# Kernel optimization log

Measured on AMD Instinct MI355X. Metric: run time of the kernel, lower is better.

## Reference

```python
import jax, jax.numpy as jnp
import numpy as np

T, H, I, E, TOP_K = 2048, 1024, 768, 8, 2


def setup_inputs() -> dict:
    key = jax.random.key(0)
    kx, kg, ku, kd, kr = jax.random.split(key, 5)
    scale_h = 1.0 / np.sqrt(H)
    scale_i = 1.0 / np.sqrt(I)
    x = jax.random.normal(kx, (T, H), dtype=jnp.float32)
    gate_w = jax.random.normal(kg, (E, I, H), dtype=jnp.float32) * scale_h
    up_w = jax.random.normal(ku, (E, I, H), dtype=jnp.float32) * scale_h
    down_w = jax.random.normal(kd, (E, H, I), dtype=jnp.float32) * scale_i
    # Router: top-k over random logits, softmax over selected, scatter to dense [T, E]
    logits = jax.random.normal(kr, (T, E), dtype=jnp.float32)
    top_vals, top_idx = jax.lax.top_k(logits, TOP_K)          # [T, K]
    top_w = jax.nn.softmax(top_vals, axis=-1)                 # [T, K]
    rows = jnp.arange(T)[:, None]                             # [T, 1]
    masked_routing_weights = jnp.zeros((T, E), jnp.float32).at[rows, top_idx].set(top_w)
    expert_select_count = jnp.zeros((E,), jnp.int32).at[top_idx.reshape(-1)].add(1)
    return {
        "x": x,
        "gate_w": gate_w,
        "up_w": up_w,
        "down_w": down_w,
        "masked_routing_weights": masked_routing_weights,
        "expert_select_count": expert_select_count,
    }


def reference(x, gate_w, up_w, down_w, masked_routing_weights, expert_select_count):
    # custom_moe_glu: per-expert GLU MLP, combined with masked routing weights.
    # x: [T, H]; gate_w/up_w: [E, I, H]; down_w: [E, H, I]; routing: [T, E]
    g = jnp.einsum("th,eih->tei", x, gate_w)                  # [T, E, I]
    u = jnp.einsum("th,eih->tei", x, up_w)                    # [T, E, I]
    h = jax.nn.silu(g) * u                                    # fused GLU activation
    # down projection per expert, then weighted combine over experts
    out = jnp.einsum("tei,ehi,te->th", h, down_w, masked_routing_weights)
    return out
```

## Files before the change

### kernel.cpp

```cpp
#include <hip/hip_runtime.h>
#include <hip/hip_bf16.h>

#define T_TOK 2048
#define H_DIM 1024
#define I_DIM 768
#define NEXP  8
#define WPE   6291456

typedef short bf16x8  __attribute__((ext_vector_type(8)));
typedef short short4v __attribute__((ext_vector_type(4)));
typedef float f32x4   __attribute__((ext_vector_type(4)));

__device__ __forceinline__ short f2bf(float f) {
  __bf16 b = (__bf16)f;
  return __builtin_bit_cast(short, b);
}
__device__ __forceinline__ void gload16(const void* g, void* l) {
  __builtin_amdgcn_global_load_lds(
      (const __attribute__((address_space(1))) void*)g,
      (__attribute__((address_space(3))) void*)l, 16, 0, 0);
}
__device__ __forceinline__ int padcnt(int c) { return (c + 127) & ~127; }
__device__ __forceinline__ int ebase(const int* __restrict__ cnts, int e) {
  int b = 0;
#pragma unroll
  for (int i = 0; i < NEXP; ++i)
    if (i < e) b += padcnt(cnts[i]);
  return b;
}


__global__ __launch_bounds__(512) void compact_k(const float* __restrict__ routw,
                                                 int* __restrict__ wsI) {
  __shared__ int sc[8];
  int e = blockIdx.x, lane = threadIdx.x & 63, w = threadIdx.x >> 6;
  unsigned long long mk[4];
  int cnt = 0;
#pragma unroll
  for (int c = 0; c < 4; ++c) {
    int tk = w * 256 + c * 64 + lane;
    float v = routw[(size_t)tk * NEXP + e];
    mk[c] = __ballot(v > 0.f);
    cnt += __popcll(mk[c]);
  }
  if (lane == 0) sc[w] = cnt;
  __syncthreads();
  int run = 0;
#pragma unroll
  for (int j = 0; j < 8; ++j)
    if (j < w) run += sc[j];
#pragma unroll
  for (int c = 0; c < 4; ++c) {
    int tk = w * 256 + c * 64 + lane;
    if ((mk[c] >> lane) & 1ull) {
      int pos = __popcll(mk[c] & ((1ull << lane) - 1));
      wsI[64 + e * T_TOK + run + pos] = tk;
    }
    run += __popcll(mk[c]);
  }
  if (w == 7 && lane == 0) wsI[e] = run;
}

__global__ __launch_bounds__(256) void gatherconv_k(const float* __restrict__ x,
                                                    const float* __restrict__ gw,
                                                    const float* __restrict__ uw,
                                                    const int* __restrict__ wsI,
                                                    unsigned short* __restrict__ xc,
                                                    unsigned short* __restrict__ wbf) {
  int bid = blockIdx.x;
  if (bid < 4096) {
    int e = bid >> 9, rb = bid & 511;
    int cnt = wsI[e];
    int pad = padcnt(cnt);
    int r = rb * 4 + (threadIdx.x >> 6);
    if (r >= pad) return;
    int base = ebase(wsI, e);
    int col = (threadIdx.x & 63) * 16;
    unsigned short* dst = xc + (size_t)(base + r) * H_DIM + col;
    if (r < cnt) {
      int tok = wsI[64 + e * T_TOK + r];
      const float* sr = x + (size_t)tok * H_DIM + col;
#pragma unroll
      for (int j = 0; j < 4; ++j) {
        float4 v = *(const float4*)(sr + j * 4);
        short4v b = {f2bf(v.x), f2bf(v.y), f2bf(v.z), f2bf(v.w)};
        *(short4v*)(dst + j * 4) = b;
      }
    } else {
#pragma unroll
      for (int j = 0; j < 4; ++j) {
        short4v z = {0, 0, 0, 0};
        *(short4v*)(dst + j * 4) = z;
      }
    }
  } else {
    size_t off = ((size_t)(bid - 4096) * 256 + threadIdx.x) * 16;
    int a = (off >= (size_t)WPE) ? 1 : 0;
    size_t rem = off - (size_t)a * WPE;
    const float* s = (a ? uw : gw) + rem;
    unsigned short* o = wbf + (size_t)a * WPE + rem;
#pragma unroll
    for (int j = 0; j < 4; ++j) {
      float4 v = *(const float4*)(s + j * 4);
      short4v b = {f2bf(v.x), f2bf(v.y), f2bf(v.z), f2bf(v.w)};
      *(short4v*)(o + j * 4) = b;
    }
  }
}

#define WB(v)                                              \
  do {                                                     \
    asm volatile("s_waitcnt vmcnt(" #v ")" ::: "memory");  \
    __builtin_amdgcn_s_barrier();                          \
    __builtin_amdgcn_sched_barrier(0);                     \
  } while (0)

__global__ __launch_bounds__(512, 2) void gemm1_k(
    const unsigned short* __restrict__ xc, unsigned short* __restrict__ wbf,
    const int* __restrict__ wsI, unsigned short* __restrict__ h,
    const float* __restrict__ dw, float* __restrict__ out) {
  int bid = blockIdx.x;
  if (bid >= 768) {
    if (bid < 1536) {
      size_t off = ((size_t)(bid - 768) * 512 + threadIdx.x) * 16;
      const float* s = dw + off;
      unsigned short* o = wbf + 2 * (size_t)WPE + off;
#pragma unroll
      for (int j = 0; j < 4; ++j) {
        float4 v = *(const float4*)(s + j * 4);
        short4v b = {f2bf(v.x), f2bf(v.y), f2bf(v.z), f2bf(v.w)};
        *(short4v*)(o + j * 4) = b;
      }
    } else {
      size_t off = ((size_t)(bid - 1536) * 512 + threadIdx.x) * 16;
      f32x4 z = {0.f, 0.f, 0.f, 0.f};
#pragma unroll
      for (int j = 0; j < 4; ++j) *(f32x4*)(out + off + j * 4) = z;
    }
    return;
  }
  int e = bid & 7, rr = bid >> 3;
  int mt = rr & 15, nt = rr >> 4;
  int cnt = wsI[e];
  int m0 = mt * 128;
  if (m0 >= cnt) return;
  int base = ebase(wsI, e);
  int n0 = nt * 128;

  __shared__ unsigned short ls[5][12288];

  int tid = threadIdx.x, lane = tid & 63, w = tid >> 6;
  int wm = w >> 2, wn = w & 3;
  int fr = lane & 15, fg = lane >> 4;
  int srow = lane >> 2;
  int scol = ((lane & 3) ^ (srow & 3)) * 8;

  const unsigned short* srcA = xc + (size_t)(base + m0 + 16 * w + srow) * H_DIM + scol;
  const unsigned short* srcG = wbf + (size_t)(e * I_DIM + n0 + 16 * w + srow) * H_DIM + scol;
  const unsigned short* srcU = wbf + WPE + (size_t)(e * I_DIM + n0 + 16 * w + srow) * H_DIM + scol;

  int roA[4], roB[4];
#pragma unroll
  for (int m = 0; m < 4; ++m) {
    int r2 = wm * 64 + m * 16 + fr;
    roA[m] = r2 * 32 + ((fg ^ (r2 & 3)) << 3);
  }
#pragma unroll
  for (int n = 0; n < 4; ++n) {
    int r2 = (n < 2) ? (wn * 32 + n * 16 + fr) : (128 + wn * 32 + (n - 2) * 16 + fr);
    roB[n] = 4096 + r2 * 32 + ((fg ^ (r2 & 3)) << 3);
  }

  bf16x8 af[2][4], bv[2][4];
  f32x4 acc[4][4] = {};

#define STG1(hh)                                                     \
  do {                                                               \
    unsigned short* lb = &ls[(hh) % 5][0];                           \
    gload16(srcA + (hh) * 32, lb + w * 512);                         \
    gload16(srcG + (hh) * 32, lb + 4096 + w * 512);                  \
    gload16(srcU + (hh) * 32, lb + 4096 + (w + 8) * 512);            \
  } while (0)
#define LDF1(st, hh)                                                 \
  do {                                                               \
    const unsigned short* lb = &ls[(hh) % 5][0];                     \
    _Pragma("unroll") for (int m = 0; m < 4; ++m) af[st][m] = *(const bf16x8*)(lb + roA[m]); \
    _Pragma("unroll") for (int n = 0; n < 4; ++n) bv[st][n] = *(const bf16x8*)(lb + roB[n]); \
  } while (0)
#define MM1(st)                                                      \
  do {                                                               \
    __builtin_amdgcn_s_setprio(1);                                   \
    _Pragma("unroll") for (int m = 0; m < 4; ++m)                    \
      _Pragma("unroll") for (int n = 0; n < 4; ++n)                  \
        acc[m][n] = __builtin_amdgcn_mfma_f32_16x16x32_bf16(af[st][m], bv[st][n], acc[m][n], 0, 0, 0); \
    __builtin_amdgcn_s_setprio(0);                                   \
  } while (0)

  STG1(0); STG1(1); STG1(2); STG1(3);
  WB(6);
  LDF1(0, 0);
#pragma unroll
  for (int i = 0; i < 32; ++i) {
    if (i + 4 < 32) STG1(i + 4);
    if (i + 1 < 32) LDF1((i + 1) & 1, i + 1);
    MM1(i & 1);
    if (i <= 27)      WB(6);
    else if (i == 28) WB(3);
    else if (i == 29) WB(0);
  }
#undef STG1
#undef LDF1
#undef MM1

#pragma unroll
  for (int m = 0; m < 4; ++m)
#pragma unroll
    for (int j = 0; j < 4; ++j) {
      int row = wm * 64 + m * 16 + fg * 4 + j;
      size_t rb2 = (size_t)(base + m0 + row) * I_DIM + n0;
#pragma unroll
      for (int jn = 0; jn < 2; ++jn) {
        float g = acc[m][jn][j];
        float u = acc[m][jn + 2][j];
        h[rb2 + wn * 32 + jn * 16 + fr] = (unsigned short)f2bf(g * u / (1.f + __expf(-g)));
      }
    }
}

__global__ __launch_bounds__(512, 2) void gemm2_k(
    const unsigned short* __restrict__ h, const unsigned short* __restrict__ wbf,
    const int* __restrict__ wsI, const float* __restrict__ routw,
    float* __restrict__ out) {
  int e = blockIdx.x & 7, rr = blockIdx.x >> 3;
  int mt = rr & 15, nt = rr >> 4;
  int cnt = wsI[e];
  int m0 = mt * 128;
  if (m0 >= cnt) return;
  int base = ebase(wsI, e);
  int n0 = nt * 256;
  const unsigned short* down_bf = wbf + 2 * (size_t)WPE;

  __shared__ unsigned short ls[5][12288];

  int tid = threadIdx.x, lane = tid & 63, w = tid >> 6;
  int wm = w >> 2, wn = w & 3;
  int fr = lane & 15, fg = lane >> 4;
  int srow = lane >> 2;
  int scol = ((lane & 3) ^ (srow & 3)) * 8;

  const unsigned short* srcA  = h + (size_t)(base + m0 + 16 * w + srow) * I_DIM + scol;
  const unsigned short* srcB1 = down_bf + (size_t)(e * H_DIM + n0 + 16 * w + srow) * I_DIM + scol;
  const unsigned short* srcB2 = down_bf + (size_t)(e * H_DIM + n0 + 16 * (w + 8) + srow) * I_DIM + scol;

  int roA[4], roB[4];
#pragma unroll
  for (int m = 0; m < 4; ++m) {
    int r2 = wm * 64 + m * 16 + fr;
    roA[m] = r2 * 32 + ((fg ^ (r2 & 3)) << 3);
  }
#pragma unroll
  for (int n = 0; n < 4; ++n) {
    int r2 = wn * 64 + n * 16 + fr;
    roB[n] = 4096 + r2 * 32 + ((fg ^ (r2 & 3)) << 3);
  }

  bf16x8 af[2][4], bv[2][4];
  f32x4 acc[4][4] = {};

#define STG2(hh)                                                     \
  do {                                                               \
    unsigned short* lb = &ls[(hh) % 5][0];                           \
    gload16(srcA + (hh) * 32, lb + w * 512);                         \
    gload16(srcB1 + (hh) * 32, lb + 4096 + w * 512);                 \
    gload16(srcB2 + (hh) * 32, lb + 4096 + (w + 8) * 512);           \
  } while (0)
#define LDF2(st, hh)                                                 \
  do {                                                               \
    const unsigned short* lb = &ls[(hh) % 5][0];                     \
    _Pragma("unroll") for (int m = 0; m < 4; ++m) af[st][m] = *(const bf16x8*)(lb + roA[m]); \
    _Pragma("unroll") for (int n = 0; n < 4; ++n) bv[st][n] = *(const bf16x8*)(lb + roB[n]); \
  } while (0)
#define MM2(st)                                                      \
  do {                                                               \
    __builtin_amdgcn_s_setprio(1);                                   \
    _Pragma("unroll") for (int m = 0; m < 4; ++m)                    \
      _Pragma("unroll") for (int n = 0; n < 4; ++n)                  \
        acc[m][n] = __builtin_amdgcn_mfma_f32_16x16x32_bf16(af[st][m], bv[st][n], acc[m][n], 0, 0, 0); \
    __builtin_amdgcn_s_setprio(0);                                   \
  } while (0)

  STG2(0); STG2(1); STG2(2); STG2(3);
  WB(6);
  LDF2(0, 0);
#pragma unroll
  for (int i = 0; i < 24; ++i) {
    if (i + 4 < 24) STG2(i + 4);
    if (i + 1 < 24) LDF2((i + 1) & 1, i + 1);
    MM2(i & 1);
    if (i <= 19)      WB(6);
    else if (i == 20) WB(3);
    else if (i == 21) WB(0);
  }
#undef STG2
#undef LDF2
#undef MM2

#pragma unroll
  for (int m = 0; m < 4; ++m)
#pragma unroll
    for (int j = 0; j < 4; ++j) {
      int row = wm * 64 + m * 16 + fg * 4 + j;
      int grow = m0 + row;
      if (grow < cnt) {
        int tk = wsI[64 + e * T_TOK + grow];
        float rw = routw[(size_t)tk * NEXP + e];
        float* orow = out + (size_t)tk * H_DIM + n0 + wn * 64;
#pragma unroll
        for (int n = 0; n < 4; ++n)
          atomicAdd(orow + n * 16 + fr, acc[m][n][j] * rw);
      }
    }
}

extern "C" void kernel_launch(void* const* d_in, const int* in_sizes, int n_in,
                              void* d_out, int out_size, void* d_ws, size_t ws_size,
                              hipStream_t stream) {
  const float* x      = (const float*)d_in[0];
  const float* gate_w = (const float*)d_in[1];
  const float* up_w   = (const float*)d_in[2];
  const float* down_w = (const float*)d_in[3];
  const float* routw  = (const float*)d_in[4];
  float* out = (float*)d_out;
  int* wsI = (int*)d_ws;

  unsigned short* wbf = (unsigned short*)((char*)d_ws + 131072);
  unsigned short* xc  = (unsigned short*)((char*)d_ws + 37879808);
  unsigned short* h   = (unsigned short*)((char*)d_ws + 48365568);

  compact_k<<<8, 512, 0, stream>>>(routw, wsI);
  gatherconv_k<<<7168, 256, 0, stream>>>(x, gate_w, up_w, wsI, xc, wbf);
  gemm1_k<<<1792, 512, 0, stream>>>(xc, wbf, wsI, h, down_w, out);
  gemm2_k<<<512, 512, 0, stream>>>(h, wbf, wsI, routw, out);
}
```

Measured before the change: 87.19 us.

## Shrink GEMM tiles to 64 rows with 2-wave blocks and simple double buffering

Both expert GEMMs move from 512-thread blocks with 128-row tiles and a 5-stage LDS pipeline to 128-thread blocks with 64-row tiles and a two-buffer loop synchronised by __syncthreads. Expert padding drops from 128 to 64 rows, which cuts wasted work on padded rows and gives more blocks to fill the GPU. The LDS swizzle gains an extra XOR term to reduce bank conflicts. In exchange the shallower pipeline and smaller tiles give less latency hiding and less operand reuse per block, and the extra blocks add more global traffic.

```diff
diff --git a/kernel.cpp b/kernel.cpp
--- a/kernel.cpp
+++ b/kernel.cpp
@@ -20,13 +20,16 @@
       (const __attribute__((address_space(1))) void*)g,
       (__attribute__((address_space(3))) void*)l, 16, 0, 0);
 }
-__device__ __forceinline__ int padcnt(int c) { return (c + 127) & ~127; }
+__device__ __forceinline__ int padcnt(int c) { return (c + 63) & ~63; }
 __device__ __forceinline__ int ebase(const int* __restrict__ cnts, int e) {
   int b = 0;
 #pragma unroll
   for (int i = 0; i < NEXP; ++i)
     if (i < e) b += padcnt(cnts[i]);
   return b;
+}
+__device__ __forceinline__ int swz(int row, int g) {
+  return g ^ (row & 3) ^ ((row >> 2) & 1);
 }
 
 
@@ -108,21 +111,15 @@
   }
 }
 
-#define WB(v)                                              \
-  do {                                                     \
-    asm volatile("s_waitcnt vmcnt(" #v ")" ::: "memory");  \
-    __builtin_amdgcn_s_barrier();                          \
-    __builtin_amdgcn_sched_barrier(0);                     \
-  } while (0)
-
-__global__ __launch_bounds__(512, 2) void gemm1_k(
+__global__ __launch_bounds__(128, 3) void gemm1_k(
     const unsigned short* __restrict__ xc, unsigned short* __restrict__ wbf,
     const int* __restrict__ wsI, unsigned short* __restrict__ h,
     const float* __restrict__ dw, float* __restrict__ out) {
   int bid = blockIdx.x;
-  if (bid >= 768) {
-    if (bid < 1536) {
-      size_t off = ((size_t)(bid - 768) * 512 + threadIdx.x) * 16;
+  int tid = threadIdx.x;
+  if (bid >= 3072) {
+    if (bid < 6144) {
+      size_t off = ((size_t)(bid - 3072) * 128 + tid) * 16;
       const float* s = dw + off;
       unsigned short* o = wbf + 2 * (size_t)WPE + off;
 #pragma unroll
@@ -132,7 +129,7 @@
         *(short4v*)(o + j * 4) = b;
       }
     } else {
-      size_t off = ((size_t)(bid - 1536) * 512 + threadIdx.x) * 16;
+      size_t off = ((size_t)(bid - 6144) * 128 + tid) * 16;
       f32x4 z = {0.f, 0.f, 0.f, 0.f};
 #pragma unroll
       for (int j = 0; j < 4; ++j) *(f32x4*)(out + off + j * 4) = z;
@@ -140,181 +137,183 @@
     return;
   }
   int e = bid & 7, rr = bid >> 3;
-  int mt = rr & 15, nt = rr >> 4;
+  int mt = rr & 31, nt = rr >> 5;
   int cnt = wsI[e];
-  int m0 = mt * 128;
+  int m0 = mt * 64;
   if (m0 >= cnt) return;
   int base = ebase(wsI, e);
-  int n0 = nt * 128;
-
-  __shared__ unsigned short ls[5][12288];
-
-  int tid = threadIdx.x, lane = tid & 63, w = tid >> 6;
-  int wm = w >> 2, wn = w & 3;
+  int g0 = nt * 64;
+
+  __shared__ unsigned short ls[2][6144];
+
+  int lane = tid & 63, w = tid >> 6;
   int fr = lane & 15, fg = lane >> 4;
   int srow = lane >> 2;
-  int scol = ((lane & 3) ^ (srow & 3)) * 8;
-
-  const unsigned short* srcA = xc + (size_t)(base + m0 + 16 * w + srow) * H_DIM + scol;
-  const unsigned short* srcG = wbf + (size_t)(e * I_DIM + n0 + 16 * w + srow) * H_DIM + scol;
-  const unsigned short* srcU = wbf + WPE + (size_t)(e * I_DIM + n0 + 16 * w + srow) * H_DIM + scol;
+  int scol = swz(srow, lane & 3) * 8;
+
+  const unsigned short* gate_bf = wbf;
+  const unsigned short* up_bf   = wbf + WPE;
+
+  const unsigned short* srcA[2];
+  const unsigned short* srcB[4];
+  int ldA[2], ldB[4];
+#pragma unroll
+  for (int i = 0; i < 2; ++i) {
+    int c = w + 2 * i;
+    ldA[i] = c * 512;
+    srcA[i] = xc + (size_t)(base + m0 + 16 * c + srow) * H_DIM + scol;
+  }
+#pragma unroll
+  for (int i = 0; i < 4; ++i) {
+    int c = w + 2 * i;
+    ldB[i] = 2048 + c * 512;
+    srcB[i] = ((c < 4) ? gate_bf + (size_t)(e * I_DIM + g0 + 16 * c + srow) * H_DIM
+                       : up_bf   + (size_t)(e * I_DIM + g0 + 16 * (c - 4) + srow) * H_DIM) + scol;
+  }
 
   int roA[4], roB[4];
 #pragma unroll
   for (int m = 0; m < 4; ++m) {
-    int r2 = wm * 64 + m * 16 + fr;
-    roA[m] = r2 * 32 + ((fg ^ (r2 & 3)) << 3);
+    int r2 = m * 16 + fr;
+    roA[m] = r2 * 32 + (swz(r2, fg) << 3);
   }
 #pragma unroll
   for (int n = 0; n < 4; ++n) {
-    int r2 = (n < 2) ? (wn * 32 + n * 16 + fr) : (128 + wn * 32 + (n - 2) * 16 + fr);
-    roB[n] = 4096 + r2 * 32 + ((fg ^ (r2 & 3)) << 3);
-  }
-
-  bf16x8 af[2][4], bv[2][4];
+    int r2 = (n < 2) ? (w * 32 + n * 16 + fr) : (64 + w * 32 + (n - 2) * 16 + fr);
+    roB[n] = 2048 + r2 * 32 + (swz(r2, fg) << 3);
+  }
+
   f32x4 acc[4][4] = {};
 
-#define STG1(hh)                                                     \
-  do {                                                               \
-    unsigned short* lb = &ls[(hh) % 5][0];                           \
-    gload16(srcA + (hh) * 32, lb + w * 512);                         \
-    gload16(srcG + (hh) * 32, lb + 4096 + w * 512);                  \
-    gload16(srcU + (hh) * 32, lb + 4096 + (w + 8) * 512);            \
+#define STG1(buf, k)                                        \
+  do {                                                      \
+    _Pragma("unroll") for (int i = 0; i < 2; ++i)           \
+      gload16(srcA[i] + (k) * 32, &ls[buf][ldA[i]]);        \
+    _Pragma("unroll") for (int i = 0; i < 4; ++i)           \
+      gload16(srcB[i] + (k) * 32, &ls[buf][ldB[i]]);        \
   } while (0)
-#define LDF1(st, hh)                                                 \
-  do {                                                               \
-    const unsigned short* lb = &ls[(hh) % 5][0];                     \
-    _Pragma("unroll") for (int m = 0; m < 4; ++m) af[st][m] = *(const bf16x8*)(lb + roA[m]); \
-    _Pragma("unroll") for (int n = 0; n < 4; ++n) bv[st][n] = *(const bf16x8*)(lb + roB[n]); \
-  } while (0)
-#define MM1(st)                                                      \
-  do {                                                               \
-    __builtin_amdgcn_s_setprio(1);                                   \
-    _Pragma("unroll") for (int m = 0; m < 4; ++m)                    \
-      _Pragma("unroll") for (int n = 0; n < 4; ++n)                  \
-        acc[m][n] = __builtin_amdgcn_mfma_f32_16x16x32_bf16(af[st][m], bv[st][n], acc[m][n], 0, 0, 0); \
-    __builtin_amdgcn_s_setprio(0);                                   \
-  } while (0)
-
-  STG1(0); STG1(1); STG1(2); STG1(3);
-  WB(6);
-  LDF1(0, 0);
-#pragma unroll
-  for (int i = 0; i < 32; ++i) {
-    if (i + 4 < 32) STG1(i + 4);
-    if (i + 1 < 32) LDF1((i + 1) & 1, i + 1);
-    MM1(i & 1);
-    if (i <= 27)      WB(6);
-    else if (i == 28) WB(3);
-    else if (i == 29) WB(0);
+
+  STG1(0, 0);
+  __syncthreads();
+  for (int k = 0; k < 32; ++k) {
+    int cur = k & 1;
+    if (k + 1 < 32) STG1(cur ^ 1, k + 1);
+    bf16x8 af[4], bv[4];
+#pragma unroll
+    for (int m = 0; m < 4; ++m) af[m] = *(const bf16x8*)&ls[cur][roA[m]];
+#pragma unroll
+    for (int n = 0; n < 4; ++n) bv[n] = *(const bf16x8*)&ls[cur][roB[n]];
+#pragma unroll
+    for (int m = 0; m < 4; ++m)
+#pragma unroll
+      for (int n = 0; n < 4; ++n)
+        acc[m][n] = __builtin_amdgcn_mfma_f32_16x16x32_bf16(af[m], bv[n], acc[m][n], 0, 0, 0);
+    __syncthreads();
   }
 #undef STG1
-#undef LDF1
-#undef MM1
 
 #pragma unroll
   for (int m = 0; m < 4; ++m)
 #pragma unroll
     for (int j = 0; j < 4; ++j) {
-      int row = wm * 64 + m * 16 + fg * 4 + j;
-      size_t rb2 = (size_t)(base + m0 + row) * I_DIM + n0;
+      int row = m * 16 + fg * 4 + j;
+      size_t rb2 = (size_t)(base + m0 + row) * I_DIM + g0;
 #pragma unroll
       for (int jn = 0; jn < 2; ++jn) {
         float g = acc[m][jn][j];
         float u = acc[m][jn + 2][j];
-        h[rb2 + wn * 32 + jn * 16 + fr] = (unsigned short)f2bf(g * u / (1.f + __expf(-g)));
-      }
-    }
-}
-
-__global__ __launch_bounds__(512, 2) void gemm2_k(
+        h[rb2 + w * 32 + jn * 16 + fr] = (unsigned short)f2bf(g * u / (1.f + __expf(-g)));
+      }
+    }
+}
+
+__global__ __launch_bounds__(128, 3) void gemm2_k(
     const unsigned short* __restrict__ h, const unsigned short* __restrict__ wbf,
     const int* __restrict__ wsI, const float* __restrict__ routw,
     float* __restrict__ out) {
   int e = blockIdx.x & 7, rr = blockIdx.x >> 3;
-  int mt = rr & 15, nt = rr >> 4;
+  int mt = rr & 31, nt = rr >> 5;
   int cnt = wsI[e];
-  int m0 = mt * 128;
+  int m0 = mt * 64;
   if (m0 >= cnt) return;
   int base = ebase(wsI, e);
-  int n0 = nt * 256;
+  int n0 = nt * 128;
   const unsigned short* down_bf = wbf + 2 * (size_t)WPE;
 
-  __shared__ unsigned short ls[5][12288];
+  __shared__ unsigned short ls[2][6144];
 
   int tid = threadIdx.x, lane = tid & 63, w = tid >> 6;
-  int wm = w >> 2, wn = w & 3;
   int fr = lane & 15, fg = lane >> 4;
   int srow = lane >> 2;
-  int scol = ((lane & 3) ^ (srow & 3)) * 8;
-
-  const unsigned short* srcA  = h + (size_t)(base + m0 + 16 * w + srow) * I_DIM + scol;
-  const unsigned short* srcB1 = down_bf + (size_t)(e * H_DIM + n0 + 16 * w + srow) * I_DIM + scol;
-  const unsigned short* srcB2 = down_bf + (size_t)(e * H_DIM + n0 + 16 * (w + 8) + srow) * I_DIM + scol;
+  int scol = swz(srow, lane & 3) * 8;
+
+  const unsigned short* srcA[2];
+  const unsigned short* srcB[4];
+  int ldA[2], ldB[4];
+#pragma unroll
+  for (int i = 0; i < 2; ++i) {
+    int c = w + 2 * i;
+    ldA[i] = c * 512;
+    srcA[i] = h + (size_t)(base + m0 + 16 * c + srow) * I_DIM + scol;
+  }
+#pragma unroll
+  for (int i = 0; i < 4; ++i) {
+    int c = w + 2 * i;
+    ldB[i] = 2048 + c * 512;
+    srcB[i] = down_bf + (size_t)(e * H_DIM + n0 + 16 * c + srow) * I_DIM + scol;
+  }
 
   int roA[4], roB[4];
 #pragma unroll
   for (int m = 0; m < 4; ++m) {
-    int r2 = wm * 64 + m * 16 + fr;
-    roA[m] = r2 * 32 + ((fg ^ (r2 & 3)) << 3);
+    int r2 = m * 16 + fr;
+    roA[m] = r2 * 32 + (swz(r2, fg) << 3);
   }
 #pragma unroll
   for (int n = 0; n < 4; ++n) {
-    int r2 = wn * 64 + n * 16 + fr;
-    roB[n] = 4096 + r2 * 32 + ((fg ^ (r2 & 3)) << 3);
-  }
-
-  bf16x8 af[2][4], bv[2][4];
+    int r2 = w * 64 + n * 16 + fr;
+    roB[n] = 2048 + r2 * 32 + (swz(r2, fg) << 3);
+  }
+
   f32x4 acc[4][4] = {};
 
-#define STG2(hh)                                                     \
-  do {                                                               \
-    unsigned short* lb = &ls[(hh) % 5][0];                           \
-    gload16(srcA + (hh) * 32, lb + w * 512);                         \
-    gload16(srcB1 + (hh) * 32, lb + 4096 + w * 512);                 \
-    gload16(srcB2 + (hh) * 32, lb + 4096 + (w + 8) * 512);           \
+#define STG2(buf, k)                                        \
+  do {                                                      \
+    _Pragma("unroll") for (int i = 0; i < 2; ++i)           \
+      gload16(srcA[i] + (k) * 32, &ls[buf][ldA[i]]);        \
+    _Pragma("unroll") for (int i = 0; i < 4; ++i)           \
+      gload16(srcB[i] + (k) * 32, &ls[buf][ldB[i]]);        \
   } while (0)
-#define LDF2(st, hh)                                                 \
-  do {                                                               \
-    const unsigned short* lb = &ls[(hh) % 5][0];                     \
-    _Pragma("unroll") for (int m = 0; m < 4; ++m) af[st][m] = *(const bf16x8*)(lb + roA[m]); \
-    _Pragma("unroll") for (int n = 0; n < 4; ++n) bv[st][n] = *(const bf16x8*)(lb + roB[n]); \
-  } while (0)
-#define MM2(st)                                                      \
-  do {                                                               \
-    __builtin_amdgcn_s_setprio(1);                                   \
-    _Pragma("unroll") for (int m = 0; m < 4; ++m)                    \
-      _Pragma("unroll") for (int n = 0; n < 4; ++n)                  \
-        acc[m][n] = __builtin_amdgcn_mfma_f32_16x16x32_bf16(af[st][m], bv[st][n], acc[m][n], 0, 0, 0); \
-    __builtin_amdgcn_s_setprio(0);                                   \
-  } while (0)
-
-  STG2(0); STG2(1); STG2(2); STG2(3);
-  WB(6);
-  LDF2(0, 0);
-#pragma unroll
-  for (int i = 0; i < 24; ++i) {
-    if (i + 4 < 24) STG2(i + 4);
-    if (i + 1 < 24) LDF2((i + 1) & 1, i + 1);
-    MM2(i & 1);
-    if (i <= 19)      WB(6);
-    else if (i == 20) WB(3);
-    else if (i == 21) WB(0);
+
+  STG2(0, 0);
+  __syncthreads();
+  for (int k = 0; k < 24; ++k) {
+    int cur = k & 1;
+    if (k + 1 < 24) STG2(cur ^ 1, k + 1);
+    bf16x8 af[4], bv[4];
+#pragma unroll
+    for (int m = 0; m < 4; ++m) af[m] = *(const bf16x8*)&ls[cur][roA[m]];
+#pragma unroll
+    for (int n = 0; n < 4; ++n) bv[n] = *(const bf16x8*)&ls[cur][roB[n]];
+#pragma unroll
+    for (int m = 0; m < 4; ++m)
+#pragma unroll
+      for (int n = 0; n < 4; ++n)
+        acc[m][n] = __builtin_amdgcn_mfma_f32_16x16x32_bf16(af[m], bv[n], acc[m][n], 0, 0, 0);
+    __syncthreads();
   }
 #undef STG2
-#undef LDF2
-#undef MM2
 
 #pragma unroll
   for (int m = 0; m < 4; ++m)
 #pragma unroll
     for (int j = 0; j < 4; ++j) {
-      int row = wm * 64 + m * 16 + fg * 4 + j;
+      int row = m * 16 + fg * 4 + j;
       int grow = m0 + row;
       if (grow < cnt) {
         int tk = wsI[64 + e * T_TOK + grow];
         float rw = routw[(size_t)tk * NEXP + e];
-        float* orow = out + (size_t)tk * H_DIM + n0 + wn * 64;
+        float* orow = out + (size_t)tk * H_DIM + n0 + w * 64;
 #pragma unroll
         for (int n = 0; n < 4; ++n)
           atomicAdd(orow + n * 16 + fr, acc[m][n][j] * rw);
@@ -339,6 +338,6 @@
 
   compact_k<<<8, 512, 0, stream>>>(routw, wsI);
   gatherconv_k<<<7168, 256, 0, stream>>>(x, gate_w, up_w, wsI, xc, wbf);
-  gemm1_k<<<1792, 512, 0, stream>>>(xc, wbf, wsI, h, down_w, out);
-  gemm2_k<<<512, 512, 0, stream>>>(h, wbf, wsI, routw, out);
-}
+  gemm1_k<<<7168, 128, 0, stream>>>(xc, wbf, wsI, h, down_w, out);
+  gemm2_k<<<2048, 128, 0, stream>>>(h, wbf, wsI, routw, out);
+}
```

After: 98.47 us. 12.9% more time.

## Move down-weight conversion and output zeroing into pre-kernel; refine LDS swizzle

Applied to the files above, without the earlier changes.

The down_w fp32-to-bf16 conversion and the zeroing of the output move out of the gemm1 launch (extra blocks) and into the preprocessing kernel, so gemm1 launches only its 768 GEMM tiles. The LDS XOR swizzle gains an extra bit from the row index (bit 2), which is meant to cut bank conflicts on fragment reads in both GEMMs. The tradeoff is a longer pre-kernel on the critical path, where before that conversion work overlapped with gemm1's compute blocks.

```diff
diff --git a/kernel.cpp b/kernel.cpp
--- a/kernel.cpp
+++ b/kernel.cpp
@@ -61,21 +61,23 @@
   if (w == 7 && lane == 0) wsI[e] = run;
 }
 
-__global__ __launch_bounds__(256) void gatherconv_k(const float* __restrict__ x,
-                                                    const float* __restrict__ gw,
-                                                    const float* __restrict__ uw,
-                                                    const int* __restrict__ wsI,
-                                                    unsigned short* __restrict__ xc,
-                                                    unsigned short* __restrict__ wbf) {
-  int bid = blockIdx.x;
+__global__ __launch_bounds__(256) void pre_k(const float* __restrict__ x,
+                                             const float* __restrict__ gw,
+                                             const float* __restrict__ uw,
+                                             const float* __restrict__ dw,
+                                             const int* __restrict__ wsI,
+                                             unsigned short* __restrict__ xc,
+                                             unsigned short* __restrict__ wbf,
+                                             float* __restrict__ out) {
+  int bid = blockIdx.x, tid = threadIdx.x;
   if (bid < 4096) {
     int e = bid >> 9, rb = bid & 511;
     int cnt = wsI[e];
     int pad = padcnt(cnt);
-    int r = rb * 4 + (threadIdx.x >> 6);
+    int r = rb * 4 + (tid >> 6);
     if (r >= pad) return;
     int base = ebase(wsI, e);
-    int col = (threadIdx.x & 63) * 16;
+    int col = (tid & 63) * 16;
     unsigned short* dst = xc + (size_t)(base + r) * H_DIM + col;
     if (r < cnt) {
       int tok = wsI[64 + e * T_TOK + r];
@@ -93,11 +95,11 @@
         *(short4v*)(dst + j * 4) = z;
       }
     }
-  } else {
-    size_t off = ((size_t)(bid - 4096) * 256 + threadIdx.x) * 16;
-    int a = (off >= (size_t)WPE) ? 1 : 0;
+  } else if (bid < 8704) {
+    size_t off = ((size_t)(bid - 4096) * 256 + tid) * 16;
+    int a = (int)(off / (size_t)WPE);
     size_t rem = off - (size_t)a * WPE;
-    const float* s = (a ? uw : gw) + rem;
+    const float* s = ((a == 0) ? gw : (a == 1) ? uw : dw) + rem;
     unsigned short* o = wbf + (size_t)a * WPE + rem;
 #pragma unroll
     for (int j = 0; j < 4; ++j) {
@@ -105,6 +107,11 @@
       short4v b = {f2bf(v.x), f2bf(v.y), f2bf(v.z), f2bf(v.w)};
       *(short4v*)(o + j * 4) = b;
     }
+  } else {
+    size_t off = ((size_t)(bid - 8704) * 256 + tid) * 16;
+    f32x4 z = {0.f, 0.f, 0.f, 0.f};
+#pragma unroll
+    for (int j = 0; j < 4; ++j) *(f32x4*)(out + off + j * 4) = z;
   }
 }
 
@@ -116,30 +123,9 @@
   } while (0)
 
 __global__ __launch_bounds__(512, 2) void gemm1_k(
-    const unsigned short* __restrict__ xc, unsigned short* __restrict__ wbf,
-    const int* __restrict__ wsI, unsigned short* __restrict__ h,
-    const float* __restrict__ dw, float* __restrict__ out) {
-  int bid = blockIdx.x;
-  if (bid >= 768) {
-    if (bid < 1536) {
-      size_t off = ((size_t)(bid - 768) * 512 + threadIdx.x) * 16;
-      const float* s = dw + off;
-      unsigned short* o = wbf + 2 * (size_t)WPE + off;
-#pragma unroll
-      for (int j = 0; j < 4; ++j) {
-        float4 v = *(const float4*)(s + j * 4);
-        short4v b = {f2bf(v.x), f2bf(v.y), f2bf(v.z), f2bf(v.w)};
-        *(short4v*)(o + j * 4) = b;
-      }
-    } else {
-      size_t off = ((size_t)(bid - 1536) * 512 + threadIdx.x) * 16;
-      f32x4 z = {0.f, 0.f, 0.f, 0.f};
-#pragma unroll
-      for (int j = 0; j < 4; ++j) *(f32x4*)(out + off + j * 4) = z;
-    }
-    return;
-  }
-  int e = bid & 7, rr = bid >> 3;
+    const unsigned short* __restrict__ xc, const unsigned short* __restrict__ wbf,
+    const int* __restrict__ wsI, unsigned short* __restrict__ h) {
+  int e = blockIdx.x & 7, rr = blockIdx.x >> 3;
   int mt = rr & 15, nt = rr >> 4;
   int cnt = wsI[e];
   int m0 = mt * 128;
@@ -153,22 +139,20 @@
   int wm = w >> 2, wn = w & 3;
   int fr = lane & 15, fg = lane >> 4;
   int srow = lane >> 2;
-  int scol = ((lane & 3) ^ (srow & 3)) * 8;
+  int scol = (((lane & 3) ^ (srow & 3) ^ ((srow >> 2) & 1))) * 8;
 
   const unsigned short* srcA = xc + (size_t)(base + m0 + 16 * w + srow) * H_DIM + scol;
   const unsigned short* srcG = wbf + (size_t)(e * I_DIM + n0 + 16 * w + srow) * H_DIM + scol;
   const unsigned short* srcU = wbf + WPE + (size_t)(e * I_DIM + n0 + 16 * w + srow) * H_DIM + scol;
 
+  int sl = ((fg ^ (fr & 3) ^ ((fr >> 2) & 1)) << 3);
   int roA[4], roB[4];
 #pragma unroll
-  for (int m = 0; m < 4; ++m) {
-    int r2 = wm * 64 + m * 16 + fr;
-    roA[m] = r2 * 32 + ((fg ^ (r2 & 3)) << 3);
-  }
+  for (int m = 0; m < 4; ++m) roA[m] = (wm * 64 + m * 16 + fr) * 32 + sl;
 #pragma unroll
   for (int n = 0; n < 4; ++n) {
     int r2 = (n < 2) ? (wn * 32 + n * 16 + fr) : (128 + wn * 32 + (n - 2) * 16 + fr);
-    roB[n] = 4096 + r2 * 32 + ((fg ^ (r2 & 3)) << 3);
+    roB[n] = 4096 + r2 * 32 + sl;
   }
 
   bf16x8 af[2][4], bv[2][4];
@@ -246,23 +230,18 @@
   int wm = w >> 2, wn = w & 3;
   int fr = lane & 15, fg = lane >> 4;
   int srow = lane >> 2;
-  int scol = ((lane & 3) ^ (srow & 3)) * 8;
+  int scol = (((lane & 3) ^ (srow & 3) ^ ((srow >> 2) & 1))) * 8;
 
   const unsigned short* srcA  = h + (size_t)(base + m0 + 16 * w + srow) * I_DIM + scol;
   const unsigned short* srcB1 = down_bf + (size_t)(e * H_DIM + n0 + 16 * w + srow) * I_DIM + scol;
   const unsigned short* srcB2 = down_bf + (size_t)(e * H_DIM + n0 + 16 * (w + 8) + srow) * I_DIM + scol;
 
+  int sl = ((fg ^ (fr & 3) ^ ((fr >> 2) & 1)) << 3);
   int roA[4], roB[4];
 #pragma unroll
-  for (int m = 0; m < 4; ++m) {
-    int r2 = wm * 64 + m * 16 + fr;
-    roA[m] = r2 * 32 + ((fg ^ (r2 & 3)) << 3);
-  }
-#pragma unroll
-  for (int n = 0; n < 4; ++n) {
-    int r2 = wn * 64 + n * 16 + fr;
-    roB[n] = 4096 + r2 * 32 + ((fg ^ (r2 & 3)) << 3);
-  }
+  for (int m = 0; m < 4; ++m) roA[m] = (wm * 64 + m * 16 + fr) * 32 + sl;
+#pragma unroll
+  for (int n = 0; n < 4; ++n) roB[n] = 4096 + (wn * 64 + n * 16 + fr) * 32 + sl;
 
   bf16x8 af[2][4], bv[2][4];
   f32x4 acc[4][4] = {};
@@ -338,7 +317,7 @@
   unsigned short* h   = (unsigned short*)((char*)d_ws + 48365568);
 
   compact_k<<<8, 512, 0, stream>>>(routw, wsI);
-  gatherconv_k<<<7168, 256, 0, stream>>>(x, gate_w, up_w, wsI, xc, wbf);
-  gemm1_k<<<1792, 512, 0, stream>>>(xc, wbf, wsI, h, down_w, out);
+  pre_k<<<9216, 256, 0, stream>>>(x, gate_w, up_w, down_w, wsI, xc, wbf, out);
+  gemm1_k<<<768, 512, 0, stream>>>(xc, wbf, wsI, h);
   gemm2_k<<<512, 512, 0, stream>>>(h, wbf, wsI, routw, out);
 }
```

Result: slower. 93.52 us (+7.3%).
